# Kernel tuning notes

Hardware: AMD Instinct MI355X
Metric: run time of the kernel (lower is better)

Reference implementation:

```python
import jax, jax.numpy as jnp
import numpy as np
from jax import lax

BN_EPS = 1e-5


def setup_inputs() -> dict:
    key = jax.random.key(0)
    k = jax.random.split(key, 7)
    B, H, W = 128, 224, 224
    return {
        "x": jax.random.normal(k[0], (B, 1, H, W), dtype=jnp.float32),
        "conv_w": jax.random.normal(k[1], (16, 1, 5, 5), dtype=jnp.float32) * 0.1,
        "conv_b": jax.random.normal(k[2], (16,), dtype=jnp.float32) * 0.1,
        "gamma": jax.random.uniform(k[3], (16,), dtype=jnp.float32, minval=0.5, maxval=1.5),
        "beta": jax.random.normal(k[4], (16,), dtype=jnp.float32) * 0.1,
        "run_mean": jax.random.normal(k[5], (16,), dtype=jnp.float32) * 0.1,
        "run_var": jax.random.uniform(k[6], (16,), dtype=jnp.float32, minval=0.5, maxval=1.5),
    }


def reference(x, conv_w, conv_b, gamma, beta, run_mean, run_var):
    # Conv2d(1,16,5,stride=1,padding=2): NCHW x OIHW -> NCHW
    y = lax.conv_general_dilated(
        x, conv_w, window_strides=(1, 1), padding=[(2, 2), (2, 2)],
        dimension_numbers=("NCHW", "OIHW", "NCHW"))
    y = y + conv_b[None, :, None, None]
    # BatchNorm2d(16) in inference form with running stats
    scale = gamma * lax.rsqrt(run_var + BN_EPS)
    y = y * scale[None, :, None, None] + (beta - run_mean * scale)[None, :, None, None]
    # ReLU
    y = jnp.maximum(y, 0.0)
    # MaxPool2d(kernel=2, stride=2)
    out = lax.reduce_window(y, -jnp.inf, lax.max,
                            window_dimensions=(1, 1, 2, 2),
                            window_strides=(1, 1, 2, 2),
                            padding="VALID")
    return out  # [B, 16, H/2, W/2]
```

## Files before the change

kernel.cpp:

```cpp
#include <hip/hip_runtime.h>
#include <stdint.h>

#define IMG 224
#define OUT_DIM 112
#define NCH 16
#define TILE 32
#define P_ROWS 36
#define P_COLS 36
#define P_STRIDE 48

typedef _Float16 h8t  __attribute__((ext_vector_type(8)));
typedef float    f32x4 __attribute__((ext_vector_type(4)));
typedef uint32_t u32x4 __attribute__((ext_vector_type(4)));

#define WS_B1 32

__global__ void prep_kernel(const float* __restrict__ conv_w,
                            const float* __restrict__ conv_b,
                            const float* __restrict__ gamma,
                            const float* __restrict__ beta,
                            const float* __restrict__ run_mean,
                            const float* __restrict__ run_var,
                            uint32_t* __restrict__ ws)
{
    int l = threadIdx.x;
    if (l >= 64) return;
    if (l < NCH) {
        float s = gamma[l] * rsqrtf(run_var[l] + 1e-5f);
        float t = fmaf(s, conv_b[l] - run_mean[l], beta[l]);
        ((float2*)ws)[l] = make_float2(s, t);
    }
    const int ch = l & 15;
    const int g  = l >> 4;
    const float* w = conv_w + ch * 25;

    float w0 = w[g * 5 + 0], w1 = w[g * 5 + 1], w2 = w[g * 5 + 2];
    float w3 = w[g * 5 + 3], w4 = w[g * 5 + 4];
    const float* wr4 = w + 20;
    float e0 = (2 * g + 0 < 5) ? wr4[2 * g + 0] : 0.f;
    float e1 = (2 * g + 1 < 5) ? wr4[2 * g + 1] : 0.f;

    auto p0 = __builtin_amdgcn_cvt_pkrtz(w0, w1);
    auto p1 = __builtin_amdgcn_cvt_pkrtz(w2, w3);
    auto p2 = __builtin_amdgcn_cvt_pkrtz(w4, 0.f);
    auto p3 = __builtin_amdgcn_cvt_pkrtz(e0, e1);
    ws[WS_B1 + l * 4 + 0] = __builtin_bit_cast(uint32_t, p0);
    ws[WS_B1 + l * 4 + 1] = __builtin_bit_cast(uint32_t, p1);
    ws[WS_B1 + l * 4 + 2] = __builtin_bit_cast(uint32_t, p2);
    ws[WS_B1 + l * 4 + 3] = __builtin_bit_cast(uint32_t, p3);
}

__global__ __launch_bounds__(256)
void conv_bn_relu_pool(const float* __restrict__ x,
                       const uint32_t* __restrict__ ws,
                       float* __restrict__ out)
{
    __shared__ uint32_t P[P_ROWS * P_STRIDE];

    const int tid = threadIdx.x;
    const int b  = blockIdx.z;
    const int ty = blockIdx.y * TILE;
    const int tx = blockIdx.x * TILE;
    const float* xb = x + (size_t)b * IMG * IMG;

    for (int i = tid; i < P_ROWS * P_STRIDE; i += 256) {
        int r = i / P_STRIDE, c = i - r * P_STRIDE;
        float v0 = 0.f, v1 = 0.f;
        int gy = ty - 2 + r;
        int gx = tx - 2 + c;
        if (c < P_COLS && (unsigned)gy < IMG) {
            const float* row = xb + gy * IMG;
            if ((unsigned)gx < IMG) v0 = row[gx];
            if ((unsigned)(gx + 1) < IMG) v1 = row[gx + 1];
        }
        auto p = __builtin_amdgcn_cvt_pkrtz(v0, v1);
        P[i] = __builtin_bit_cast(uint32_t, p);
    }

    const int lane = tid & 63;
    const int wv   = tid >> 6;
    const int pp   = lane & 15;
    const int g    = lane >> 4;

    u32x4 b1u = *(const u32x4*)(ws + WS_B1 + lane * 4);
    h8t  B1 = __builtin_bit_cast(h8t, b1u);
    float2 sst = ((const float2*)ws)[pp];

    __syncthreads();

    float* outb = out + ((size_t)b * NCH + pp) * (OUT_DIM * OUT_DIM);

    for (int s = 0; s < 4; ++s) {
        const int yl = 8 * wv + 2 * s;
        const int oy = (ty >> 1) + 4 * wv + s;
        #pragma unroll
        for (int sub = 0; sub < 2; ++sub) {
            const int cb = sub * 16 + pp;
            const uint32_t* rA = P + (yl + g) * P_STRIDE + cb;
            const uint32_t* r4 = P + (yl + 4) * P_STRIDE + cb + 2*g;

            f32x4 accA = {0.f, 0.f, 0.f, 0.f};
            f32x4 accB = {0.f, 0.f, 0.f, 0.f};

            u32x4 a1 = {rA[0], rA[2], rA[4], r4[0]};
            accA = __builtin_amdgcn_mfma_f32_16x16x32_f16(
                       __builtin_bit_cast(h8t, a1), B1, accA, 0, 0, 0);
            u32x4 c1 = {rA[P_STRIDE], rA[P_STRIDE + 2], rA[P_STRIDE + 4], r4[P_STRIDE]};
            accB = __builtin_amdgcn_mfma_f32_16x16x32_f16(
                       __builtin_bit_cast(h8t, c1), B1, accB, 0, 0, 0);

            float m0 = fmaxf(fmaxf(accA[0], accA[1]), fmaxf(accB[0], accB[1]));
            float m1 = fmaxf(fmaxf(accA[2], accA[3]), fmaxf(accB[2], accB[3]));
            float y0 = fmaxf(fmaf(m0, sst.x, sst.y), 0.f);
            float y1 = fmaxf(fmaf(m1, sst.x, sst.y), 0.f);

            const int ox = (tx >> 1) + sub * 8 + 2 * g;
            *(float2*)(outb + oy * OUT_DIM + ox) = make_float2(y0, y1);
        }
    }
}

extern "C" void kernel_launch(void* const* d_in, const int* in_sizes, int n_in,
                              void* d_out, int out_size, void* d_ws, size_t ws_size,
                              hipStream_t stream) {
    const float* x        = (const float*)d_in[0];
    const float* conv_w   = (const float*)d_in[1];
    const float* conv_b   = (const float*)d_in[2];
    const float* gamma    = (const float*)d_in[3];
    const float* beta     = (const float*)d_in[4];
    const float* run_mean = (const float*)d_in[5];
    const float* run_var  = (const float*)d_in[6];
    float* out = (float*)d_out;
    uint32_t* ws = (uint32_t*)d_ws;

    prep_kernel<<<1, 64, 0, stream>>>(conv_w, conv_b, gamma, beta, run_mean, run_var, ws);

    dim3 grid(IMG / TILE, IMG / TILE, 128);
    dim3 block(256);
    conv_bn_relu_pool<<<grid, block, 0, stream>>>(x, ws, out);
}
```

Baseline: 172.2 us.

## Use full-width row-strip tiles with parity-split fp16 LDS layout and inline weight prep

Replaces 32x32 tiles with 16-row strips that span the full image width, which removes horizontal halo redundancy and shrinks the grid. Input is staged into LDS as two packed-fp16 copies, one even-aligned and one odd-aligned, so MFMA operand gathers read contiguous words. The separate prep kernel is removed and every block computes its own fp16 weight fragments and BN scale/shift, saving one launch at the cost of redundant per-block work. Each wave now issues 14 column subtiles per row pair instead of 2.

```diff
diff --git a/kernel.cpp b/kernel.cpp
--- a/kernel.cpp
+++ b/kernel.cpp
@@ -4,118 +4,95 @@
 #define IMG 224
 #define OUT_DIM 112
 #define NCH 16
-#define TILE 32
-#define P_ROWS 36
-#define P_COLS 36
-#define P_STRIDE 48
+#define TILE_Y 16
+#define R_ROWS 20
+#define HJ 116
+#define HSZ (R_ROWS * HJ)
 
 typedef _Float16 h8t  __attribute__((ext_vector_type(8)));
 typedef float    f32x4 __attribute__((ext_vector_type(4)));
 typedef uint32_t u32x4 __attribute__((ext_vector_type(4)));
 
-#define WS_B1 32
-
-__global__ void prep_kernel(const float* __restrict__ conv_w,
-                            const float* __restrict__ conv_b,
-                            const float* __restrict__ gamma,
-                            const float* __restrict__ beta,
-                            const float* __restrict__ run_mean,
-                            const float* __restrict__ run_var,
-                            uint32_t* __restrict__ ws)
-{
-    int l = threadIdx.x;
-    if (l >= 64) return;
-    if (l < NCH) {
-        float s = gamma[l] * rsqrtf(run_var[l] + 1e-5f);
-        float t = fmaf(s, conv_b[l] - run_mean[l], beta[l]);
-        ((float2*)ws)[l] = make_float2(s, t);
-    }
-    const int ch = l & 15;
-    const int g  = l >> 4;
-    const float* w = conv_w + ch * 25;
-
-    float w0 = w[g * 5 + 0], w1 = w[g * 5 + 1], w2 = w[g * 5 + 2];
-    float w3 = w[g * 5 + 3], w4 = w[g * 5 + 4];
-    const float* wr4 = w + 20;
-    float e0 = (2 * g + 0 < 5) ? wr4[2 * g + 0] : 0.f;
-    float e1 = (2 * g + 1 < 5) ? wr4[2 * g + 1] : 0.f;
-
-    auto p0 = __builtin_amdgcn_cvt_pkrtz(w0, w1);
-    auto p1 = __builtin_amdgcn_cvt_pkrtz(w2, w3);
-    auto p2 = __builtin_amdgcn_cvt_pkrtz(w4, 0.f);
-    auto p3 = __builtin_amdgcn_cvt_pkrtz(e0, e1);
-    ws[WS_B1 + l * 4 + 0] = __builtin_bit_cast(uint32_t, p0);
-    ws[WS_B1 + l * 4 + 1] = __builtin_bit_cast(uint32_t, p1);
-    ws[WS_B1 + l * 4 + 2] = __builtin_bit_cast(uint32_t, p2);
-    ws[WS_B1 + l * 4 + 3] = __builtin_bit_cast(uint32_t, p3);
-}
-
 __global__ __launch_bounds__(256)
 void conv_bn_relu_pool(const float* __restrict__ x,
-                       const uint32_t* __restrict__ ws,
+                       const float* __restrict__ conv_w,
+                       const float* __restrict__ conv_b,
+                       const float* __restrict__ gamma,
+                       const float* __restrict__ beta,
+                       const float* __restrict__ run_mean,
+                       const float* __restrict__ run_var,
                        float* __restrict__ out)
 {
-    __shared__ uint32_t P[P_ROWS * P_STRIDE];
+    __shared__ uint32_t H[2 * HSZ];
 
     const int tid = threadIdx.x;
-    const int b  = blockIdx.z;
-    const int ty = blockIdx.y * TILE;
-    const int tx = blockIdx.x * TILE;
+    const int b   = blockIdx.y;
+    const int ty  = blockIdx.x * TILE_Y;
     const float* xb = x + (size_t)b * IMG * IMG;
-
-    for (int i = tid; i < P_ROWS * P_STRIDE; i += 256) {
-        int r = i / P_STRIDE, c = i - r * P_STRIDE;
-        float v0 = 0.f, v1 = 0.f;
-        int gy = ty - 2 + r;
-        int gx = tx - 2 + c;
-        if (c < P_COLS && (unsigned)gy < IMG) {
-            const float* row = xb + gy * IMG;
-            if ((unsigned)gx < IMG) v0 = row[gx];
-            if ((unsigned)(gx + 1) < IMG) v1 = row[gx + 1];
-        }
-        auto p = __builtin_amdgcn_cvt_pkrtz(v0, v1);
-        P[i] = __builtin_bit_cast(uint32_t, p);
-    }
 
     const int lane = tid & 63;
     const int wv   = tid >> 6;
     const int pp   = lane & 15;
     const int g    = lane >> 4;
 
-    u32x4 b1u = *(const u32x4*)(ws + WS_B1 + lane * 4);
-    h8t  B1 = __builtin_bit_cast(h8t, b1u);
-    float2 sst = ((const float2*)ws)[pp];
+    const float* w = conv_w + pp * 25;
+    float w0 = w[g*5+0], w1 = w[g*5+1], w2 = w[g*5+2], w3 = w[g*5+3], w4 = w[g*5+4];
+    float e0 = (2*g   < 5) ? w[20 + 2*g]     : 0.f;
+    float e1 = (2*g+1 < 5) ? w[20 + 2*g + 1] : 0.f;
+    u32x4 bu;
+    bu[0] = __builtin_bit_cast(uint32_t, __builtin_amdgcn_cvt_pkrtz(w0, w1));
+    bu[1] = __builtin_bit_cast(uint32_t, __builtin_amdgcn_cvt_pkrtz(w2, w3));
+    bu[2] = __builtin_bit_cast(uint32_t, __builtin_amdgcn_cvt_pkrtz(w4, 0.f));
+    bu[3] = __builtin_bit_cast(uint32_t, __builtin_amdgcn_cvt_pkrtz(e0, e1));
+    h8t B1 = __builtin_bit_cast(h8t, bu);
+    float sc = gamma[pp] * rsqrtf(run_var[pp] + 1e-5f);
+    float sh = fmaf(sc, conv_b[pp] - run_mean[pp], beta[pp]);
 
+    for (int i = tid; i < HSZ; i += 256) {
+        int r = i / HJ, j = i - r * HJ;
+        int gy = ty - 2 + r;
+        int c  = 2 * j;
+        float v0 = 0.f, v1 = 0.f, v2 = 0.f;
+        if ((unsigned)gy < IMG) {
+            const float* row = xb + gy * IMG;
+            if ((unsigned)(c - 2) < IMG) v0 = row[c - 2];
+            if ((unsigned)(c - 1) < IMG) v1 = row[c - 1];
+            if ((unsigned)(c    ) < IMG) v2 = row[c];
+        }
+        H[i]       = __builtin_bit_cast(uint32_t, __builtin_amdgcn_cvt_pkrtz(v0, v1));
+        H[HSZ + i] = __builtin_bit_cast(uint32_t, __builtin_amdgcn_cvt_pkrtz(v1, v2));
+    }
     __syncthreads();
 
+    const uint32_t* Hq = H + (pp & 1) * HSZ + (pp >> 1);
     float* outb = out + ((size_t)b * NCH + pp) * (OUT_DIM * OUT_DIM);
 
-    for (int s = 0; s < 4; ++s) {
-        const int yl = 8 * wv + 2 * s;
-        const int oy = (ty >> 1) + 4 * wv + s;
+    #pragma unroll
+    for (int s = 0; s < 2; ++s) {
+        const int y0 = 4 * wv + 2 * s;
+        const int oy = blockIdx.x * 8 + 2 * wv + s;
+        const uint32_t* rA = Hq + (y0 + g) * HJ;
+        const uint32_t* r4 = Hq + (y0 + 4) * HJ + g;
+        float* orow = outb + oy * OUT_DIM + 2 * g;
+
         #pragma unroll
-        for (int sub = 0; sub < 2; ++sub) {
-            const int cb = sub * 16 + pp;
-            const uint32_t* rA = P + (yl + g) * P_STRIDE + cb;
-            const uint32_t* r4 = P + (yl + 4) * P_STRIDE + cb + 2*g;
-
+        for (int sub = 0; sub < 14; ++sub) {
+            const int j0 = sub * 8;
             f32x4 accA = {0.f, 0.f, 0.f, 0.f};
             f32x4 accB = {0.f, 0.f, 0.f, 0.f};
 
-            u32x4 a1 = {rA[0], rA[2], rA[4], r4[0]};
+            u32x4 a1 = { rA[j0], rA[j0 + 1], rA[j0 + 2], r4[j0] };
             accA = __builtin_amdgcn_mfma_f32_16x16x32_f16(
                        __builtin_bit_cast(h8t, a1), B1, accA, 0, 0, 0);
-            u32x4 c1 = {rA[P_STRIDE], rA[P_STRIDE + 2], rA[P_STRIDE + 4], r4[P_STRIDE]};
+            u32x4 c1 = { rA[j0 + HJ], rA[j0 + 1 + HJ], rA[j0 + 2 + HJ], r4[j0 + HJ] };
             accB = __builtin_amdgcn_mfma_f32_16x16x32_f16(
                        __builtin_bit_cast(h8t, c1), B1, accB, 0, 0, 0);
 
             float m0 = fmaxf(fmaxf(accA[0], accA[1]), fmaxf(accB[0], accB[1]));
             float m1 = fmaxf(fmaxf(accA[2], accA[3]), fmaxf(accB[2], accB[3]));
-            float y0 = fmaxf(fmaf(m0, sst.x, sst.y), 0.f);
-            float y1 = fmaxf(fmaf(m1, sst.x, sst.y), 0.f);
-
-            const int ox = (tx >> 1) + sub * 8 + 2 * g;
-            *(float2*)(outb + oy * OUT_DIM + ox) = make_float2(y0, y1);
+            float y0v = fmaxf(fmaf(m0, sc, sh), 0.f);
+            float y1v = fmaxf(fmaf(m1, sc, sh), 0.f);
+            *(float2*)(orow + sub * 8) = make_float2(y0v, y1v);
         }
     }
 }
@@ -131,11 +108,9 @@
     const float* run_mean = (const float*)d_in[5];
     const float* run_var  = (const float*)d_in[6];
     float* out = (float*)d_out;
-    uint32_t* ws = (uint32_t*)d_ws;
 
-    prep_kernel<<<1, 64, 0, stream>>>(conv_w, conv_b, gamma, beta, run_mean, run_var, ws);
-
-    dim3 grid(IMG / TILE, IMG / TILE, 128);
+    dim3 grid(IMG / TILE_Y, 128);
     dim3 block(256);
-    conv_bn_relu_pool<<<grid, block, 0, stream>>>(x, ws, out);
+    conv_bn_relu_pool<<<grid, block, 0, stream>>>(
+        x, conv_w, conv_b, gamma, beta, run_mean, run_var, out);
 }
```

Result: faster. 153.3 us (-11.0%).
